# Kernel optimization log

Measured on AMD Instinct MI355X. Metric: run time of the kernel, lower is better.

The kernel has to match this reference:

```python
import jax, jax.numpy as jnp
import numpy as np

N0, N1, N2, N3 = 600000, 100000, 10000, 1000
E0, E1, E2 = 1000000, 100000, 10000
DIN, DH, DOUT = 128, 256, 47


def _glorot(k, fan_in, fan_out):
    s = np.sqrt(2.0 / (fan_in + fan_out)).astype(np.float32)
    return jax.random.normal(k, (fan_in, fan_out), jnp.float32) * s


def setup_inputs() -> dict:
    key = jax.random.key(0)
    ks = jax.random.split(key, 13)
    return {
        "x": jax.random.normal(ks[0], (N0, DIN), jnp.float32),
        "src0": jax.random.randint(ks[1], (E0,), 0, N0, jnp.int32),
        "dst0": jax.random.randint(ks[2], (E0,), 0, N1, jnp.int32),
        "src1": jax.random.randint(ks[3], (E1,), 0, N1, jnp.int32),
        "dst1": jax.random.randint(ks[4], (E1,), 0, N2, jnp.int32),
        "src2": jax.random.randint(ks[5], (E2,), 0, N2, jnp.int32),
        "dst2": jax.random.randint(ks[6], (E2,), 0, N3, jnp.int32),
        "Wl0": _glorot(ks[7], DIN, DH), "Wr0": _glorot(ks[8], DIN, DH),
        "b0": jnp.zeros((DH,), jnp.float32),
        "Wl1": _glorot(ks[9], DH, DH), "Wr1": _glorot(ks[10], DH, DH),
        "b1": jnp.zeros((DH,), jnp.float32),
        "Wl2": _glorot(ks[11], DH, DOUT), "Wr2": _glorot(ks[12], DH, DOUT),
        "b2": jnp.zeros((DOUT,), jnp.float32),
        "size1": N1, "size2": N2, "size3": N3,
    }


def _sage_conv(x, src, dst, n_tgt, Wl, Wr, b):
    # PyG SAGEConv (mean aggr, root_weight=True, bias in lin_l) on a bipartite
    # sampled subgraph: x_src = x (all frontier nodes), x_tgt = x[:n_tgt].
    msgs = x[src]                                   # [E, Din] gather
    agg = jax.ops.segment_sum(msgs, dst, num_segments=n_tgt)
    cnt = jax.ops.segment_sum(jnp.ones((dst.shape[0],), x.dtype), dst,
                              num_segments=n_tgt)
    mean = agg / jnp.maximum(cnt, 1.0)[:, None]     # [n_tgt, Din]
    return mean @ Wl + b + x[:n_tgt] @ Wr           # [n_tgt, Dout]


def reference(x, src0, dst0, src1, dst1, src2, dst2,
              Wl0, Wr0, b0, Wl1, Wr1, b1, Wl2, Wr2, b2,
              size1, size2, size3):
    # layer 0
    h = jax.nn.relu(_sage_conv(x, src0, dst0, size1, Wl0, Wr0, b0))
    # dropout(p=0.5) is identity in eval mode
    # layer 1
    h = jax.nn.relu(_sage_conv(h, src1, dst1, size2, Wl1, Wr1, b1))
    # layer 2 (no relu/dropout)
    h = _sage_conv(h, src2, dst2, size3, Wl2, Wr2, b2)
    return jax.nn.log_softmax(h, axis=-1)           # [size3, out_channels]
```

## Files before the change

kernel.cpp:

```cpp
#include <hip/hip_runtime.h>
#include <cstdint>
#include <cstddef>
#include <cmath>

#define N0C 600000
#define N1C 100000
#define N2C 10000
#define N3C 1000
#define E0C 1000000
#define E1C 100000
#define E2C 10000

typedef unsigned short u16;
typedef unsigned int u32;
typedef __attribute__((ext_vector_type(8))) short bf16x8;
typedef __attribute__((ext_vector_type(4))) float f32x4;

__device__ __forceinline__ u16 f2b(float x) {
  u32 u = __builtin_bit_cast(u32, x);
  u32 r = (u + 0x7fffu + ((u >> 16) & 1u)) >> 16;
  return (u16)r;
}
__device__ __forceinline__ float b2f(u16 h) {
  u32 u = ((u32)h) << 16;
  return __builtin_bit_cast(float, u);
}

__global__ __launch_bounds__(256) void hist_kernel(
    const int* __restrict__ dst, int E, int* __restrict__ cnt) {
  int i = blockIdx.x * blockDim.x + threadIdx.x;
  if (i < E) atomicAdd(&cnt[dst[i]], 1);
}

__global__ __launch_bounds__(256) void scan_block(
    int* __restrict__ data, int n, int* __restrict__ partials) {
  __shared__ int sdata[256];
  const int t = threadIdx.x;
  const int base = blockIdx.x * 1024;
  const int idx = base + t * 4;
  int v[4];
  int sum = 0;
#pragma unroll
  for (int k = 0; k < 4; k++) {
    int x = (idx + k < n) ? data[idx + k] : 0;
    v[k] = x; sum += x;
  }
  sdata[t] = sum;
  __syncthreads();
  for (int off = 1; off < 256; off <<= 1) {
    int x = (t >= off) ? sdata[t - off] : 0;
    __syncthreads();
    sdata[t] += x;
    __syncthreads();
  }
  int run = (t > 0) ? sdata[t - 1] : 0;
#pragma unroll
  for (int k = 0; k < 4; k++) {
    run += v[k];
    if (idx + k < n) data[idx + k] = run;
  }
  if (t == 255) partials[blockIdx.x] = sdata[255];
}

__global__ __launch_bounds__(1024) void scan_partials(int* __restrict__ partials, int nb) {
  __shared__ int sdata[1024];
  const int t = threadIdx.x;
  sdata[t] = (t < nb) ? partials[t] : 0;
  __syncthreads();
  for (int off = 1; off < 1024; off <<= 1) {
    int x = (t >= off) ? sdata[t - off] : 0;
    __syncthreads();
    sdata[t] += x;
    __syncthreads();
  }
  int ex = (t > 0) ? sdata[t - 1] : 0;
  if (t < nb) partials[t] = ex;
}

__global__ __launch_bounds__(256) void add_offsets(
    const int* __restrict__ incl, const int* __restrict__ partials, int n,
    int* __restrict__ off) {
  int i = blockIdx.x * blockDim.x + threadIdx.x;
  if (i < n) off[i + 1] = incl[i] + partials[i >> 10];
  if (i == 0) off[0] = 0;
}

__global__ __launch_bounds__(256) void fill_kernel(
    const int* __restrict__ src, const int* __restrict__ dst, int E,
    const int* __restrict__ off, int* __restrict__ cur, int* __restrict__ esrc) {
  int i = blockIdx.x * blockDim.x + threadIdx.x;
  if (i < E) {
    int d = dst[i];
    int p = atomicAdd(&cur[d], 1);
    esrc[off[d] + p] = src[i];
  }
}

__global__ __launch_bounds__(256) void cvt_f32_bf16(
    const float* __restrict__ in, u16* __restrict__ out, int n4) {
  int i = blockIdx.x * blockDim.x + threadIdx.x;
  if (i < n4) {
    float4 v = *(const float4*)(in + (size_t)i * 4);
    ushort4 o;
    o.x = f2b(v.x); o.y = f2b(v.y); o.z = f2b(v.z); o.w = f2b(v.w);
    *(ushort4*)(out + (size_t)i * 4) = o;
  }
}

__global__ __launch_bounds__(256) void cvt_wt(
    const float* __restrict__ Wl, const float* __restrict__ Wr, int Kh,
    u16* __restrict__ Wt) {
  int Ktot = 2 * Kh;
  int idx = blockIdx.x * blockDim.x + threadIdx.x;
  if (idx >= 256 * Ktot) return;
  int n = idx / Ktot, k = idx - n * Ktot;
  float v = (k < Kh) ? Wl[(size_t)k * 256 + n] : Wr[(size_t)(k - Kh) * 256 + n];
  Wt[idx] = f2b(v);
}

__global__ __launch_bounds__(256) void gather128_bf16(
    const float* __restrict__ X, const int* __restrict__ off,
    const int* __restrict__ esrc, int Nt, u16* __restrict__ mean) {
  int w = (blockIdx.x * blockDim.x + threadIdx.x) >> 6;
  int lane = threadIdx.x & 63;
  if (w >= Nt) return;
  int s = off[w], e = off[w + 1];
  float ax = 0.f, ay = 0.f;
  int j = s;
  for (; j + 1 < e; j += 2) {
    int s0 = esrc[j], s1 = esrc[j + 1];
    float2 v0 = *(const float2*)(X + (size_t)s0 * 128 + lane * 2);
    float2 v1 = *(const float2*)(X + (size_t)s1 * 128 + lane * 2);
    ax += v0.x + v1.x; ay += v0.y + v1.y;
  }
  if (j < e) {
    int s0 = esrc[j];
    float2 v0 = *(const float2*)(X + (size_t)s0 * 128 + lane * 2);
    ax += v0.x; ay += v0.y;
  }
  float inv = 1.0f / fmaxf((float)(e - s), 1.0f);
  u32 p = ((u32)f2b(ay * inv) << 16) | (u32)f2b(ax * inv);
  ((u32*)(mean + (size_t)w * 128))[lane] = p;
}

__global__ __launch_bounds__(256) void gather256_bf16(
    const u16* __restrict__ X, const int* __restrict__ off,
    const int* __restrict__ esrc, int Nt, u16* __restrict__ mean) {
  int w = (blockIdx.x * blockDim.x + threadIdx.x) >> 6;
  int lane = threadIdx.x & 63;
  if (w >= Nt) return;
  int s = off[w], e = off[w + 1];
  float a0 = 0.f, a1 = 0.f, a2 = 0.f, a3 = 0.f;
  int j = s;
  for (; j + 1 < e; j += 2) {
    int s0 = esrc[j], s1 = esrc[j + 1];
    ushort4 v0 = *(const ushort4*)(X + (size_t)s0 * 256 + lane * 4);
    ushort4 v1 = *(const ushort4*)(X + (size_t)s1 * 256 + lane * 4);
    a0 += b2f(v0.x) + b2f(v1.x); a1 += b2f(v0.y) + b2f(v1.y);
    a2 += b2f(v0.z) + b2f(v1.z); a3 += b2f(v0.w) + b2f(v1.w);
  }
  if (j < e) {
    int s0 = esrc[j];
    ushort4 v0 = *(const ushort4*)(X + (size_t)s0 * 256 + lane * 4);
    a0 += b2f(v0.x); a1 += b2f(v0.y); a2 += b2f(v0.z); a3 += b2f(v0.w);
  }
  float inv = 1.0f / fmaxf((float)(e - s), 1.0f);
  ushort4 o;
  o.x = f2b(a0 * inv); o.y = f2b(a1 * inv); o.z = f2b(a2 * inv); o.w = f2b(a3 * inv);
  *(ushort4*)(mean + (size_t)w * 256 + lane * 4) = o;
}

__global__ __launch_bounds__(256) void gemm_mfma(
    const u16* __restrict__ A1, const u16* __restrict__ A2, int Kh,
    const u16* __restrict__ Wt, const float* __restrict__ bias,
    u16* __restrict__ C, int M, int do_relu) {
  const int tid = threadIdx.x;
  const int wave = tid >> 6, lane = tid & 63;
  const int lr = lane & 15, quad = lane >> 4;
  const int wr = wave >> 1, wc = wave & 1;
  const int rowBase = blockIdx.x * 128 + wr * 64;
  const int colBase = blockIdx.y * 128 + wc * 64;
  const int Ktot = 2 * Kh;

  f32x4 acc[4][4] = {};

  size_t aoff[4];
#pragma unroll
  for (int mt = 0; mt < 4; mt++) {
    int r = rowBase + mt * 16 + lr;
    if (r >= M) r = M - 1;
    aoff[mt] = (size_t)r * Kh;
  }
  const u16* wrow[4];
  float bs[4];
#pragma unroll
  for (int nt = 0; nt < 4; nt++) {
    int n = colBase + nt * 16 + lr;
    wrow[nt] = Wt + (size_t)n * Ktot;
    bs[nt] = bias[n];
  }

#pragma unroll
  for (int half = 0; half < 2; half++) {
    const u16* Asrc = half ? A2 : A1;
    const int kb = half * Kh;
    for (int kt = 0; kt < Kh; kt += 32) {
      bf16x8 af[4], bfr[4];
#pragma unroll
      for (int mt = 0; mt < 4; mt++)
        af[mt] = *(const bf16x8*)(Asrc + aoff[mt] + kt + quad * 8);
#pragma unroll
      for (int nt = 0; nt < 4; nt++)
        bfr[nt] = *(const bf16x8*)(wrow[nt] + kb + kt + quad * 8);
#pragma unroll
      for (int mt = 0; mt < 4; mt++)
#pragma unroll
        for (int nt = 0; nt < 4; nt++)
          acc[mt][nt] = __builtin_amdgcn_mfma_f32_16x16x32_bf16(
              af[mt], bfr[nt], acc[mt][nt], 0, 0, 0);
    }
  }

#pragma unroll
  for (int mt = 0; mt < 4; mt++) {
#pragma unroll
    for (int reg = 0; reg < 4; reg++) {
      int row = rowBase + mt * 16 + quad * 4 + reg;
      if (row < M) {
#pragma unroll
        for (int nt = 0; nt < 4; nt++) {
          float v = acc[mt][nt][reg] + bs[nt];
          if (do_relu) v = fmaxf(v, 0.f);
          C[(size_t)row * 256 + colBase + nt * 16 + lr] = f2b(v);
        }
      }
    }
  }
}

__global__ __launch_bounds__(64) void layer2_lsm(
    const u16* __restrict__ mean2, const u16* __restrict__ h2,
    const float* __restrict__ Wl2, const float* __restrict__ Wr2,
    const float* __restrict__ b2, float* __restrict__ out) {
  __shared__ float arow[512];
  const int i = blockIdx.x;
  const int lane = threadIdx.x;
  for (int t = lane; t < 256; t += 64) {
    arow[t] = b2f(mean2[(size_t)i * 256 + t]);
    arow[256 + t] = b2f(h2[(size_t)i * 256 + t]);
  }
  __syncthreads();
  float acc = 0.0f;
  if (lane < 47) {
    acc = b2[lane];
#pragma unroll 4
    for (int k = 0; k < 256; k++) acc += arow[k] * Wl2[k * 47 + lane];
#pragma unroll 4
    for (int k = 0; k < 256; k++) acc += arow[256 + k] * Wr2[k * 47 + lane];
  }
  float v = (lane < 47) ? acc : -INFINITY;
#pragma unroll
  for (int off = 32; off >= 1; off >>= 1) v = fmaxf(v, __shfl_xor(v, off, 64));
  float e = (lane < 47) ? expf(acc - v) : 0.0f;
  float s = e;
#pragma unroll
  for (int off = 32; off >= 1; off >>= 1) s += __shfl_xor(s, off, 64);
  if (lane < 47) out[(size_t)i * 47 + lane] = acc - v - logf(s);
}

extern "C" void kernel_launch(void* const* d_in, const int* in_sizes, int n_in,
                              void* d_out, int out_size, void* d_ws, size_t ws_size,
                              hipStream_t stream) {
  (void)in_sizes; (void)n_in; (void)out_size; (void)ws_size;
  const float* x   = (const float*)d_in[0];
  const int* src0  = (const int*)d_in[1];
  const int* dst0  = (const int*)d_in[2];
  const int* src1  = (const int*)d_in[3];
  const int* dst1  = (const int*)d_in[4];
  const int* src2  = (const int*)d_in[5];
  const int* dst2  = (const int*)d_in[6];
  const float* Wl0 = (const float*)d_in[7];
  const float* Wr0 = (const float*)d_in[8];
  const float* b0  = (const float*)d_in[9];
  const float* Wl1 = (const float*)d_in[10];
  const float* Wr1 = (const float*)d_in[11];
  const float* b1  = (const float*)d_in[12];
  const float* Wl2 = (const float*)d_in[13];
  const float* Wr2 = (const float*)d_in[14];
  const float* b2  = (const float*)d_in[15];

  char* p = (char*)d_ws;
  u16* mean0 = (u16*)p; p += (size_t)N1C * 128 * 2;
  u16* xb    = (u16*)p; p += (size_t)N1C * 128 * 2;
  u16* h1    = (u16*)p; p += (size_t)N1C * 256 * 2;
  u16* mean1 = (u16*)p; p += (size_t)N2C * 256 * 2;
  u16* h2    = (u16*)p; p += (size_t)N2C * 256 * 2;
  u16* mean2 = (u16*)p; p += (size_t)N3C * 256 * 2;
  u16* Wt0   = (u16*)p; p += (size_t)256 * 256 * 2;
  u16* Wt1   = (u16*)p; p += (size_t)256 * 512 * 2;
  int* cnt0  = (int*)p;
  int* cur0  = cnt0 + 100000;
  int* off0  = cur0 + 100000;
  int* part0 = off0 + 100256;
  int* esrc0 = part0 + 256;
  int* cnt1  = esrc0 + 1000000;
  int* cur1  = cnt1 + 10000;
  int* off1  = cur1 + 10000;
  int* part1 = off1 + 10256;
  int* esrc1 = part1 + 256;
  int* cnt2  = esrc1 + 100000;
  int* cur2  = cnt2 + 1000;
  int* off2  = cur2 + 1000;
  int* part2 = off2 + 1256;
  int* esrc2 = part2 + 256;
  float* out = (float*)d_out;

  cvt_f32_bf16<<<(N1C * 128 / 4 + 255) / 256, 256, 0, stream>>>(x, xb, N1C * 128 / 4);
  cvt_wt<<<(256 * 256 + 255) / 256, 256, 0, stream>>>(Wl0, Wr0, 128, Wt0);
  cvt_wt<<<(256 * 512 + 255) / 256, 256, 0, stream>>>(Wl1, Wr1, 256, Wt1);

  hipMemsetAsync(cnt0, 0, (size_t)200000 * 4, stream);
  hist_kernel<<<(E0C + 255) / 256, 256, 0, stream>>>(dst0, E0C, cnt0);
  scan_block<<<(N1C + 1023) / 1024, 256, 0, stream>>>(cnt0, N1C, part0);
  scan_partials<<<1, 1024, 0, stream>>>(part0, (N1C + 1023) / 1024);
  add_offsets<<<(N1C + 255) / 256, 256, 0, stream>>>(cnt0, part0, N1C, off0);
  fill_kernel<<<(E0C + 255) / 256, 256, 0, stream>>>(src0, dst0, E0C, off0, cur0, esrc0);
  gather128_bf16<<<N1C / 4, 256, 0, stream>>>(x, off0, esrc0, N1C, mean0);
  gemm_mfma<<<dim3(782, 2), 256, 0, stream>>>(mean0, xb, 128, Wt0, b0, h1, N1C, 1);

  hipMemsetAsync(cnt1, 0, (size_t)20000 * 4, stream);
  hist_kernel<<<(E1C + 255) / 256, 256, 0, stream>>>(dst1, E1C, cnt1);
  scan_block<<<(N2C + 1023) / 1024, 256, 0, stream>>>(cnt1, N2C, part1);
  scan_partials<<<1, 1024, 0, stream>>>(part1, (N2C + 1023) / 1024);
  add_offsets<<<(N2C + 255) / 256, 256, 0, stream>>>(cnt1, part1, N2C, off1);
  fill_kernel<<<(E1C + 255) / 256, 256, 0, stream>>>(src1, dst1, E1C, off1, cur1, esrc1);
  gather256_bf16<<<N2C / 4, 256, 0, stream>>>(h1, off1, esrc1, N2C, mean1);
  gemm_mfma<<<dim3(79, 2), 256, 0, stream>>>(mean1, h1, 256, Wt1, b1, h2, N2C, 1);

  hipMemsetAsync(cnt2, 0, (size_t)2000 * 4, stream);
  hist_kernel<<<(E2C + 255) / 256, 256, 0, stream>>>(dst2, E2C, cnt2);
  scan_block<<<1, 256, 0, stream>>>(cnt2, N3C, part2);
  scan_partials<<<1, 1024, 0, stream>>>(part2, 1);
  add_offsets<<<(N3C + 255) / 256, 256, 0, stream>>>(cnt2, part2, N3C, off2);
  fill_kernel<<<(E2C + 255) / 256, 256, 0, stream>>>(src2, dst2, E2C, off2, cur2, esrc2);
  gather256_bf16<<<N3C / 4, 256, 0, stream>>>(h2, off2, esrc2, N3C, mean2);
  layer2_lsm<<<N3C, 64, 0, stream>>>(mean2, h2, Wl2, Wr2, b2, out);
}
```

Measured before the change: 803.7 us.

## Batch CSR construction across layers and gather layer-0 features from bf16 copy

Merges the histogram, scan, offset and fill kernels of all three layers into single launches, and merges the two weight conversions into one, to cut launch overhead. Converts the whole 600k-row input x to bf16 so the layer-0 neighbour gather reads half-width rows. The gather loops are also unrolled by four to keep more loads in flight. In exchange, converting all of x adds a full streaming read and write, and mean aggregation now uses bf16-rounded inputs.

```diff
diff --git a/kernel.cpp b/kernel.cpp
--- a/kernel.cpp
+++ b/kernel.cpp
@@ -26,18 +26,27 @@
   return __builtin_bit_cast(float, u);
 }
 
-__global__ __launch_bounds__(256) void hist_kernel(
-    const int* __restrict__ dst, int E, int* __restrict__ cnt) {
+__global__ __launch_bounds__(256) void hist3(
+    const int* __restrict__ d0, const int* __restrict__ d1,
+    const int* __restrict__ d2, int* __restrict__ c0, int* __restrict__ c1,
+    int* __restrict__ c2) {
   int i = blockIdx.x * blockDim.x + threadIdx.x;
-  if (i < E) atomicAdd(&cnt[dst[i]], 1);
-}
-
-__global__ __launch_bounds__(256) void scan_block(
-    int* __restrict__ data, int n, int* __restrict__ partials) {
+  if (i < E0C) atomicAdd(&c0[d0[i]], 1);
+  else if (i < E0C + E1C) atomicAdd(&c1[d1[i - E0C]], 1);
+  else if (i < E0C + E1C + E2C) atomicAdd(&c2[d2[i - E0C - E1C]], 1);
+}
+
+__global__ __launch_bounds__(256) void scan_block3(
+    int* __restrict__ c0, int* __restrict__ c1, int* __restrict__ c2,
+    int* __restrict__ p0, int* __restrict__ p1, int* __restrict__ p2) {
   __shared__ int sdata[256];
+  const int b = blockIdx.x;
+  int* data; int n; int* partials; int lb;
+  if (b < 98)       { data = c0; n = N1C; partials = p0; lb = b; }
+  else if (b < 108) { data = c1; n = N2C; partials = p1; lb = b - 98; }
+  else              { data = c2; n = N3C; partials = p2; lb = b - 108; }
   const int t = threadIdx.x;
-  const int base = blockIdx.x * 1024;
-  const int idx = base + t * 4;
+  const int idx = lb * 1024 + t * 4;
   int v[4];
   int sum = 0;
 #pragma unroll
@@ -59,40 +68,66 @@
     run += v[k];
     if (idx + k < n) data[idx + k] = run;
   }
-  if (t == 255) partials[blockIdx.x] = sdata[255];
-}
-
-__global__ __launch_bounds__(1024) void scan_partials(int* __restrict__ partials, int nb) {
-  __shared__ int sdata[1024];
+  if (t == 255) partials[lb] = sdata[255];
+}
+
+__global__ __launch_bounds__(128) void scan_partials3(
+    int* __restrict__ p0, int* __restrict__ p1, int* __restrict__ p2) {
+  __shared__ int sdata[128];
+  int* p; int nb;
+  if (blockIdx.x == 0)      { p = p0; nb = 98; }
+  else if (blockIdx.x == 1) { p = p1; nb = 10; }
+  else                      { p = p2; nb = 1; }
   const int t = threadIdx.x;
-  sdata[t] = (t < nb) ? partials[t] : 0;
+  sdata[t] = (t < nb) ? p[t] : 0;
   __syncthreads();
-  for (int off = 1; off < 1024; off <<= 1) {
+  for (int off = 1; off < 128; off <<= 1) {
     int x = (t >= off) ? sdata[t - off] : 0;
     __syncthreads();
     sdata[t] += x;
     __syncthreads();
   }
   int ex = (t > 0) ? sdata[t - 1] : 0;
-  if (t < nb) partials[t] = ex;
-}
-
-__global__ __launch_bounds__(256) void add_offsets(
-    const int* __restrict__ incl, const int* __restrict__ partials, int n,
-    int* __restrict__ off) {
+  if (t < nb) p[t] = ex;
+}
+
+__global__ __launch_bounds__(256) void addoff3(
+    const int* __restrict__ c0, const int* __restrict__ c1,
+    const int* __restrict__ c2, const int* __restrict__ p0,
+    const int* __restrict__ p1, const int* __restrict__ p2,
+    int* __restrict__ o0, int* __restrict__ o1, int* __restrict__ o2) {
   int i = blockIdx.x * blockDim.x + threadIdx.x;
-  if (i < n) off[i + 1] = incl[i] + partials[i >> 10];
-  if (i == 0) off[0] = 0;
-}
-
-__global__ __launch_bounds__(256) void fill_kernel(
-    const int* __restrict__ src, const int* __restrict__ dst, int E,
-    const int* __restrict__ off, int* __restrict__ cur, int* __restrict__ esrc) {
+  if (i < N1C) {
+    o0[i + 1] = c0[i] + p0[i >> 10];
+    if (i == 0) o0[0] = 0;
+  } else if (i < N1C + N2C) {
+    int j = i - N1C;
+    o1[j + 1] = c1[j] + p1[j >> 10];
+    if (j == 0) o1[0] = 0;
+  } else if (i < N1C + N2C + N3C) {
+    int j = i - N1C - N2C;
+    o2[j + 1] = c2[j] + p2[j >> 10];
+    if (j == 0) o2[0] = 0;
+  }
+}
+
+__global__ __launch_bounds__(256) void fill3(
+    const int* __restrict__ s0, const int* __restrict__ d0,
+    const int* __restrict__ s1, const int* __restrict__ d1,
+    const int* __restrict__ s2, const int* __restrict__ d2,
+    const int* __restrict__ o0, const int* __restrict__ o1,
+    const int* __restrict__ o2, int* __restrict__ u0, int* __restrict__ u1,
+    int* __restrict__ u2, int* __restrict__ e0, int* __restrict__ e1,
+    int* __restrict__ e2) {
   int i = blockIdx.x * blockDim.x + threadIdx.x;
-  if (i < E) {
-    int d = dst[i];
-    int p = atomicAdd(&cur[d], 1);
-    esrc[off[d] + p] = src[i];
+  if (i < E0C) {
+    int d = d0[i]; int p = atomicAdd(&u0[d], 1); e0[o0[d] + p] = s0[i];
+  } else if (i < E0C + E1C) {
+    int j = i - E0C;
+    int d = d1[j]; int p = atomicAdd(&u1[d], 1); e1[o1[d] + p] = s1[j];
+  } else if (i < E0C + E1C + E2C) {
+    int j = i - E0C - E1C;
+    int d = d2[j]; int p = atomicAdd(&u2[d], 1); e2[o2[d] + p] = s2[j];
   }
 }
 
@@ -107,39 +142,49 @@
   }
 }
 
-__global__ __launch_bounds__(256) void cvt_wt(
-    const float* __restrict__ Wl, const float* __restrict__ Wr, int Kh,
-    u16* __restrict__ Wt) {
-  int Ktot = 2 * Kh;
+__global__ __launch_bounds__(256) void cvt_wt2(
+    const float* __restrict__ Wl0, const float* __restrict__ Wr0,
+    const float* __restrict__ Wl1, const float* __restrict__ Wr1,
+    u16* __restrict__ Wt0, u16* __restrict__ Wt1) {
   int idx = blockIdx.x * blockDim.x + threadIdx.x;
-  if (idx >= 256 * Ktot) return;
-  int n = idx / Ktot, k = idx - n * Ktot;
-  float v = (k < Kh) ? Wl[(size_t)k * 256 + n] : Wr[(size_t)(k - Kh) * 256 + n];
-  Wt[idx] = f2b(v);
+  if (idx < 256 * 256) {
+    int n = idx >> 8, k = idx & 255;
+    float v = (k < 128) ? Wl0[(size_t)k * 256 + n] : Wr0[(size_t)(k - 128) * 256 + n];
+    Wt0[idx] = f2b(v);
+  } else if (idx < 256 * 256 + 256 * 512) {
+    int j = idx - 256 * 256;
+    int n = j >> 9, k = j & 511;
+    float v = (k < 256) ? Wl1[(size_t)k * 256 + n] : Wr1[(size_t)(k - 256) * 256 + n];
+    Wt1[j] = f2b(v);
+  }
 }
 
 __global__ __launch_bounds__(256) void gather128_bf16(
-    const float* __restrict__ X, const int* __restrict__ off,
+    const u16* __restrict__ X, const int* __restrict__ off,
     const int* __restrict__ esrc, int Nt, u16* __restrict__ mean) {
   int w = (blockIdx.x * blockDim.x + threadIdx.x) >> 6;
   int lane = threadIdx.x & 63;
   if (w >= Nt) return;
   int s = off[w], e = off[w + 1];
-  float ax = 0.f, ay = 0.f;
+  const u32* Xr = (const u32*)X;
+  float a0 = 0.f, a1 = 0.f;
   int j = s;
-  for (; j + 1 < e; j += 2) {
-    int s0 = esrc[j], s1 = esrc[j + 1];
-    float2 v0 = *(const float2*)(X + (size_t)s0 * 128 + lane * 2);
-    float2 v1 = *(const float2*)(X + (size_t)s1 * 128 + lane * 2);
-    ax += v0.x + v1.x; ay += v0.y + v1.y;
-  }
-  if (j < e) {
-    int s0 = esrc[j];
-    float2 v0 = *(const float2*)(X + (size_t)s0 * 128 + lane * 2);
-    ax += v0.x; ay += v0.y;
+  for (; j + 3 < e; j += 4) {
+    u32 r0 = Xr[(size_t)esrc[j + 0] * 64 + lane];
+    u32 r1 = Xr[(size_t)esrc[j + 1] * 64 + lane];
+    u32 r2 = Xr[(size_t)esrc[j + 2] * 64 + lane];
+    u32 r3 = Xr[(size_t)esrc[j + 3] * 64 + lane];
+    a0 += b2f((u16)r0) + b2f((u16)r1) + b2f((u16)r2) + b2f((u16)r3);
+    a1 += b2f((u16)(r0 >> 16)) + b2f((u16)(r1 >> 16)) +
+          b2f((u16)(r2 >> 16)) + b2f((u16)(r3 >> 16));
+  }
+  for (; j < e; j++) {
+    u32 r = Xr[(size_t)esrc[j] * 64 + lane];
+    a0 += b2f((u16)r);
+    a1 += b2f((u16)(r >> 16));
   }
   float inv = 1.0f / fmaxf((float)(e - s), 1.0f);
-  u32 p = ((u32)f2b(ay * inv) << 16) | (u32)f2b(ax * inv);
+  u32 p = ((u32)f2b(a1 * inv) << 16) | (u32)f2b(a0 * inv);
   ((u32*)(mean + (size_t)w * 128))[lane] = p;
 }
 
@@ -152,16 +197,18 @@
   int s = off[w], e = off[w + 1];
   float a0 = 0.f, a1 = 0.f, a2 = 0.f, a3 = 0.f;
   int j = s;
-  for (; j + 1 < e; j += 2) {
-    int s0 = esrc[j], s1 = esrc[j + 1];
-    ushort4 v0 = *(const ushort4*)(X + (size_t)s0 * 256 + lane * 4);
-    ushort4 v1 = *(const ushort4*)(X + (size_t)s1 * 256 + lane * 4);
-    a0 += b2f(v0.x) + b2f(v1.x); a1 += b2f(v0.y) + b2f(v1.y);
-    a2 += b2f(v0.z) + b2f(v1.z); a3 += b2f(v0.w) + b2f(v1.w);
-  }
-  if (j < e) {
-    int s0 = esrc[j];
-    ushort4 v0 = *(const ushort4*)(X + (size_t)s0 * 256 + lane * 4);
+  for (; j + 3 < e; j += 4) {
+    ushort4 v0 = *(const ushort4*)(X + (size_t)esrc[j + 0] * 256 + lane * 4);
+    ushort4 v1 = *(const ushort4*)(X + (size_t)esrc[j + 1] * 256 + lane * 4);
+    ushort4 v2 = *(const ushort4*)(X + (size_t)esrc[j + 2] * 256 + lane * 4);
+    ushort4 v3 = *(const ushort4*)(X + (size_t)esrc[j + 3] * 256 + lane * 4);
+    a0 += b2f(v0.x) + b2f(v1.x) + b2f(v2.x) + b2f(v3.x);
+    a1 += b2f(v0.y) + b2f(v1.y) + b2f(v2.y) + b2f(v3.y);
+    a2 += b2f(v0.z) + b2f(v1.z) + b2f(v2.z) + b2f(v3.z);
+    a3 += b2f(v0.w) + b2f(v1.w) + b2f(v2.w) + b2f(v3.w);
+  }
+  for (; j < e; j++) {
+    ushort4 v0 = *(const ushort4*)(X + (size_t)esrc[j] * 256 + lane * 4);
     a0 += b2f(v0.x); a1 += b2f(v0.y); a2 += b2f(v0.z); a3 += b2f(v0.w);
   }
   float inv = 1.0f / fmaxf((float)(e - s), 1.0f);
@@ -290,8 +337,8 @@
   const float* b2  = (const float*)d_in[15];
 
   char* p = (char*)d_ws;
+  u16* xb    = (u16*)p; p += (size_t)N0C * 128 * 2;
   u16* mean0 = (u16*)p; p += (size_t)N1C * 128 * 2;
-  u16* xb    = (u16*)p; p += (size_t)N1C * 128 * 2;
   u16* h1    = (u16*)p; p += (size_t)N1C * 256 * 2;
   u16* mean1 = (u16*)p; p += (size_t)N2C * 256 * 2;
   u16* h2    = (u16*)p; p += (size_t)N2C * 256 * 2;
@@ -300,49 +347,43 @@
   u16* Wt1   = (u16*)p; p += (size_t)256 * 512 * 2;
   int* cnt0  = (int*)p;
   int* cur0  = cnt0 + 100000;
-  int* off0  = cur0 + 100000;
-  int* part0 = off0 + 100256;
-  int* esrc0 = part0 + 256;
-  int* cnt1  = esrc0 + 1000000;
+  int* cnt1  = cur0 + 100000;
   int* cur1  = cnt1 + 10000;
-  int* off1  = cur1 + 10000;
-  int* part1 = off1 + 10256;
-  int* esrc1 = part1 + 256;
-  int* cnt2  = esrc1 + 100000;
+  int* cnt2  = cur1 + 10000;
   int* cur2  = cnt2 + 1000;
-  int* off2  = cur2 + 1000;
-  int* part2 = off2 + 1256;
-  int* esrc2 = part2 + 256;
+  int* off0  = cur2 + 1000 + 48;
+  int* off1  = off0 + 100096;
+  int* off2  = off1 + 10112;
+  int* part0 = off2 + 1088;
+  int* part1 = part0 + 128;
+  int* part2 = part1 + 128;
+  int* esrc0 = part2 + 128;
+  int* esrc1 = esrc0 + 1000000;
+  int* esrc2 = esrc1 + 100000;
   float* out = (float*)d_out;
 
-  cvt_f32_bf16<<<(N1C * 128 / 4 + 255) / 256, 256, 0, stream>>>(x, xb, N1C * 128 / 4);
-  cvt_wt<<<(256 * 256 + 255) / 256, 256, 0, stream>>>(Wl0, Wr0, 128, Wt0);
-  cvt_wt<<<(256 * 512 + 255) / 256, 256, 0, stream>>>(Wl1, Wr1, 256, Wt1);
-
-  hipMemsetAsync(cnt0, 0, (size_t)200000 * 4, stream);
-  hist_kernel<<<(E0C + 255) / 256, 256, 0, stream>>>(dst0, E0C, cnt0);
-  scan_block<<<(N1C + 1023) / 1024, 256, 0, stream>>>(cnt0, N1C, part0);
-  scan_partials<<<1, 1024, 0, stream>>>(part0, (N1C + 1023) / 1024);
-  add_offsets<<<(N1C + 255) / 256, 256, 0, stream>>>(cnt0, part0, N1C, off0);
-  fill_kernel<<<(E0C + 255) / 256, 256, 0, stream>>>(src0, dst0, E0C, off0, cur0, esrc0);
-  gather128_bf16<<<N1C / 4, 256, 0, stream>>>(x, off0, esrc0, N1C, mean0);
+  hipMemsetAsync(cnt0, 0, (size_t)222000 * 4, stream);
+  hist3<<<(E0C + E1C + E2C + 255) / 256, 256, 0, stream>>>(
+      dst0, dst1, dst2, cnt0, cnt1, cnt2);
+  scan_block3<<<109, 256, 0, stream>>>(cnt0, cnt1, cnt2, part0, part1, part2);
+  scan_partials3<<<3, 128, 0, stream>>>(part0, part1, part2);
+  addoff3<<<(N1C + N2C + N3C + 255) / 256, 256, 0, stream>>>(
+      cnt0, cnt1, cnt2, part0, part1, part2, off0, off1, off2);
+  fill3<<<(E0C + E1C + E2C + 255) / 256, 256, 0, stream>>>(
+      src0, dst0, src1, dst1, src2, dst2, off0, off1, off2,
+      cur0, cur1, cur2, esrc0, esrc1, esrc2);
+
+  cvt_wt2<<<(256 * 256 + 256 * 512 + 255) / 256, 256, 0, stream>>>(
+      Wl0, Wr0, Wl1, Wr1, Wt0, Wt1);
+  cvt_f32_bf16<<<(N0C * 128 / 4 + 255) / 256, 256, 0, stream>>>(
+      x, xb, N0C * 128 / 4);
+
+  gather128_bf16<<<N1C / 4, 256, 0, stream>>>(xb, off0, esrc0, N1C, mean0);
   gemm_mfma<<<dim3(782, 2), 256, 0, stream>>>(mean0, xb, 128, Wt0, b0, h1, N1C, 1);
 
-  hipMemsetAsync(cnt1, 0, (size_t)20000 * 4, stream);
-  hist_kernel<<<(E1C + 255) / 256, 256, 0, stream>>>(dst1, E1C, cnt1);
-  scan_block<<<(N2C + 1023) / 1024, 256, 0, stream>>>(cnt1, N2C, part1);
-  scan_partials<<<1, 1024, 0, stream>>>(part1, (N2C + 1023) / 1024);
-  add_offsets<<<(N2C + 255) / 256, 256, 0, stream>>>(cnt1, part1, N2C, off1);
-  fill_kernel<<<(E1C + 255) / 256, 256, 0, stream>>>(src1, dst1, E1C, off1, cur1, esrc1);
   gather256_bf16<<<N2C / 4, 256, 0, stream>>>(h1, off1, esrc1, N2C, mean1);
   gemm_mfma<<<dim3(79, 2), 256, 0, stream>>>(mean1, h1, 256, Wt1, b1, h2, N2C, 1);
 
-  hipMemsetAsync(cnt2, 0, (size_t)2000 * 4, stream);
-  hist_kernel<<<(E2C + 255) / 256, 256, 0, stream>>>(dst2, E2C, cnt2);
-  scan_block<<<1, 256, 0, stream>>>(cnt2, N3C, part2);
-  scan_partials<<<1, 1024, 0, stream>>>(part2, 1);
-  add_offsets<<<(N3C + 255) / 256, 256, 0, stream>>>(cnt2, part2, N3C, off2);
-  fill_kernel<<<(E2C + 255) / 256, 256, 0, stream>>>(src2, dst2, E2C, off2, cur2, esrc2);
   gather256_bf16<<<N3C / 4, 256, 0, stream>>>(h2, off2, esrc2, N3C, mean2);
   layer2_lsm<<<N3C, 64, 0, stream>>>(mean2, h2, Wl2, Wr2, b2, out);
 }
```

New measurement: 784.5 us. -2.4%, faster.
